# Optimization experiments

Measured on AMD Instinct MI355X. Metric: run time of the kernel, lower is better.

## Reference

```python
import jax, jax.numpy as jnp
import numpy as np

D_MODEL = 1024
D_HIDDEN = 4096
NUM_EXPERTS = 8
TOP_K = 2


def setup_inputs() -> dict:
    key = jax.random.key(0)
    ks = jax.random.split(key, 7)
    scale_in = 1.0 / np.sqrt(D_MODEL)
    scale_hid = 1.0 / np.sqrt(D_HIDDEN)
    x = jax.random.normal(ks[0], (4, 2048, D_MODEL), dtype=jnp.float32)
    Wr = jax.random.uniform(ks[1], (D_MODEL, NUM_EXPERTS), jnp.float32, -scale_in, scale_in)
    br = jax.random.uniform(ks[2], (NUM_EXPERTS,), jnp.float32, -scale_in, scale_in)
    W1 = jax.random.uniform(ks[3], (NUM_EXPERTS, D_MODEL, D_HIDDEN), jnp.float32, -scale_in, scale_in)
    b1 = jax.random.uniform(ks[4], (NUM_EXPERTS, D_HIDDEN), jnp.float32, -scale_in, scale_in)
    W2 = jax.random.uniform(ks[5], (NUM_EXPERTS, D_HIDDEN, D_MODEL), jnp.float32, -scale_hid, scale_hid)
    b2 = jax.random.uniform(ks[6], (NUM_EXPERTS, D_MODEL), jnp.float32, -scale_hid, scale_hid)
    return {"x": x, "Wr": Wr, "br": br, "W1": W1, "b1": b1, "W2": W2, "b2": b2}


def reference(x, Wr, br, W1, b1, W2, b2):
    B, S, D = x.shape
    E = Wr.shape[1]
    flat = x.reshape(-1, D)                      # [T, D]
    T = flat.shape[0]
    logits = flat @ Wr + br                      # [T, E]
    probs = jax.nn.softmax(logits, axis=-1)
    topk_p, topk_i = jax.lax.top_k(probs, TOP_K)  # [T, K]
    topk_p = topk_p / jnp.sum(topk_p, axis=-1, keepdims=True)
    # combine[t, e] = sum_k topk_p[t, k] * (topk_i[t, k] == e)
    combine = jnp.zeros((T, E), flat.dtype).at[jnp.arange(T)[:, None], topk_i].add(topk_p)
    out = jnp.zeros_like(flat)
    for e in range(E):  # fixed small expert loop; each iter is a dense GEMM pair
        h = jax.nn.relu(flat @ W1[e] + b1[e])    # [T, d_hidden]
        y = h @ W2[e] + b2[e]                    # [T, D]
        out = out + y * combine[:, e:e + 1]
    return out.reshape(B, S, D)
```

## Files before the change

### kernel.cpp

```cpp
#include <hip/hip_runtime.h>
#include <stdint.h>

#define D_MODEL  1024
#define D_HIDDEN 4096
#define NE       8
#define T_TOK    8192
#define BM       128
#define BN       128
#define BK       64
#define MAXT     136
#define ROWS_CAP 17408

typedef __attribute__((ext_vector_type(8))) short short8;
typedef __attribute__((ext_vector_type(4))) float f32x4;

__device__ inline uint16_t f2bf(float f) {
  uint32_t u = __float_as_uint(f);
  uint32_t r = (u + 0x7fffu + ((u >> 16) & 1u)) >> 16;
  return (uint16_t)r;
}

#define GLOAD16(gp, lp) __builtin_amdgcn_global_load_lds( \
  (const __attribute__((address_space(1))) uint32_t*)(gp), \
  (__attribute__((address_space(3))) uint32_t*)(lp), 16, 0, 0)

__global__ void transpose_cvt(const float* __restrict__ in, uint16_t* __restrict__ out,
                              int R, int C) {
  __shared__ float tile[64][65];
  size_t eoff = (size_t)blockIdx.z * R * C;
  int c0 = blockIdx.x * 64, r0 = blockIdx.y * 64;
  int t = threadIdx.x;
  int lr = t >> 4, lc4 = (t & 15) * 4;
#pragma unroll
  for (int i = 0; i < 4; ++i) {
    int rr = i * 16 + lr;
    float4 v = *(const float4*)(in + eoff + (size_t)(r0 + rr) * C + c0 + lc4);
    tile[rr][lc4] = v.x; tile[rr][lc4 + 1] = v.y;
    tile[rr][lc4 + 2] = v.z; tile[rr][lc4 + 3] = v.w;
  }
  __syncthreads();
  int oc = t >> 3, orr = (t & 7) * 8;
#pragma unroll
  for (int i = 0; i < 2; ++i) {
    int cc = i * 32 + oc;
    short8 o;
#pragma unroll
    for (int j = 0; j < 8; ++j) o[j] = (short)f2bf(tile[orr + j][cc]);
    *(short8*)(out + eoff + (size_t)(c0 + cc) * R + r0 + orr) = o;
  }
}

__global__ void router_kernel(const float* __restrict__ x, const float* __restrict__ Wr,
                              const float* __restrict__ br,
                              int* __restrict__ cnt, int* __restrict__ tok_of,
                              int* __restrict__ k_of, float* __restrict__ tok_w) {
  int t = blockIdx.x * 4 + (threadIdx.x >> 6);
  int l = threadIdx.x & 63;
  const float* xr = x + (size_t)t * D_MODEL;
  float a[8] = {0.f,0.f,0.f,0.f,0.f,0.f,0.f,0.f};
  for (int d = l; d < D_MODEL; d += 64) {
    float xv = xr[d];
    const float4* w4 = (const float4*)(Wr + d * 8);
    float4 wa = w4[0], wb = w4[1];
    a[0] += xv * wa.x; a[1] += xv * wa.y; a[2] += xv * wa.z; a[3] += xv * wa.w;
    a[4] += xv * wb.x; a[5] += xv * wb.y; a[6] += xv * wb.z; a[7] += xv * wb.w;
  }
#pragma unroll
  for (int e = 0; e < 8; ++e) {
    float v = a[e];
#pragma unroll
    for (int off = 32; off > 0; off >>= 1) v += __shfl_xor(v, off);
    a[e] = v + br[e];
  }
  if (l == 0) {
    int i1 = 0; float v1 = a[0];
#pragma unroll
    for (int e = 1; e < 8; ++e) if (a[e] > v1) { v1 = a[e]; i1 = e; }
    int i2 = -1; float v2 = -1e30f;
#pragma unroll
    for (int e = 0; e < 8; ++e) if (e != i1 && a[e] > v2) { v2 = a[e]; i2 = e; }
    float e2 = __expf(v2 - v1);
    float inv = 1.0f / (1.0f + e2);
    int p1 = atomicAdd(cnt + i1, 1);
    tok_of[i1 * T_TOK + p1] = t; k_of[i1 * T_TOK + p1] = 0;
    int p2 = atomicAdd(cnt + i2, 1);
    tok_of[i2 * T_TOK + p2] = t; k_of[i2 * T_TOK + p2] = 1;
    tok_w[t * 2 + 0] = inv; tok_w[t * 2 + 1] = e2 * inv;
  }
}

__global__ void setup_kernel(const int* __restrict__ cnt, int* __restrict__ meta) {
  int l = threadIdx.x;
  int tiles[8], base[9], tpre[9];
  base[0] = 0; tpre[0] = 0;
#pragma unroll
  for (int e = 0; e < 8; ++e) {
    int c = cnt[e];
    tiles[e] = (c + BM - 1) / BM;
    base[e + 1] = base[e] + tiles[e] * BM;
    tpre[e + 1] = tpre[e] + tiles[e];
  }
  int nt = tpre[8];
  if (l == 0) meta[0] = nt;
  if (l < 9) meta[1 + l] = base[l];
  for (int i = l; i < nt; i += 64) {
    int e = 0;
#pragma unroll
    for (int k = 1; k < 8; ++k) if (i >= tpre[k]) e = k;
    meta[16 + i] = e;
    meta[16 + MAXT + i] = base[e] + (i - tpre[e]) * BM;
  }
}

__global__ void gather_kernel(const float* __restrict__ x, const int* __restrict__ cnt,
                              const int* __restrict__ meta, const int* __restrict__ tok_of,
                              const int* __restrict__ k_of, const float* __restrict__ tok_w,
                              uint16_t* __restrict__ xp,
                              int* __restrict__ row2tok, float* __restrict__ row2w) {
  int r = blockIdx.x * 4 + (threadIdx.x >> 6);
  int l = threadIdx.x & 63;
  int total = meta[9];
  if (r >= total) return;
  int e = 0;
#pragma unroll
  for (int i = 1; i < 8; ++i) if (r >= meta[1 + i]) e = i;
  int p = r - meta[1 + e];
  uint16_t* dst = xp + (size_t)r * D_MODEL + l * 16;
  if (p < cnt[e]) {
    int t = tok_of[e * T_TOK + p];
    if (l == 0) {
      row2tok[r] = t;
      row2w[r] = tok_w[t * 2 + k_of[e * T_TOK + p]];
    }
    const float4* src = (const float4*)(x + (size_t)t * D_MODEL + l * 16);
    short8 o0, o1;
    float4 v0 = src[0], v1 = src[1], v2 = src[2], v3 = src[3];
    o0[0] = (short)f2bf(v0.x); o0[1] = (short)f2bf(v0.y);
    o0[2] = (short)f2bf(v0.z); o0[3] = (short)f2bf(v0.w);
    o0[4] = (short)f2bf(v1.x); o0[5] = (short)f2bf(v1.y);
    o0[6] = (short)f2bf(v1.z); o0[7] = (short)f2bf(v1.w);
    o1[0] = (short)f2bf(v2.x); o1[1] = (short)f2bf(v2.y);
    o1[2] = (short)f2bf(v2.z); o1[3] = (short)f2bf(v2.w);
    o1[4] = (short)f2bf(v3.x); o1[5] = (short)f2bf(v3.y);
    o1[6] = (short)f2bf(v3.z); o1[7] = (short)f2bf(v3.w);
    *(short8*)dst = o0;
    *(short8*)(dst + 8) = o1;
  } else {
    if (l == 0) { row2tok[r] = -1; row2w[r] = 0.f; }
    short8 z = {0,0,0,0,0,0,0,0};
    *(short8*)dst = z;
    *(short8*)(dst + 8) = z;
  }
}

template<int KD, int ND, int NTX, bool FUSED_OUT>
__global__ void moe_gemm(const uint16_t* __restrict__ A, const uint16_t* __restrict__ Bt,
                         const float* __restrict__ bias,
                         uint16_t* __restrict__ Cb, float* __restrict__ out,
                         const int* __restrict__ row2tok, const float* __restrict__ row2w,
                         const int* __restrict__ meta) {
  int nt = meta[0];
  int d = blockIdx.x;
  int xcd = d & 7, q = d >> 3;
  int mt = xcd * (MAXT / 8) + q / NTX;
  if (mt >= nt) return;
  int n0 = (q % NTX) * BN;
  int e = meta[16 + mt];
  int row0 = meta[16 + MAXT + mt];

  __shared__ __align__(16) uint16_t lA[BM * BK];
  __shared__ __align__(16) uint16_t lB[BN * BK];

  int t = threadIdx.x;
  int w = t >> 6, l = t & 63;
  int wr = (w >> 1) * 64, wc = (w & 1) * 64;

  const uint16_t* Ab = A + (size_t)row0 * KD;
  const uint16_t* Bb = Bt + ((size_t)e * ND + n0) * KD;

  f32x4 acc[4][4];
#pragma unroll
  for (int m = 0; m < 4; ++m)
#pragma unroll
    for (int n = 0; n < 4; ++n) acc[m][n] = (f32x4){0.f, 0.f, 0.f, 0.f};

  int trow = t >> 3;
  int tcol = (t & 7) * 8;
  int scol = tcol ^ ((trow & 7) << 3);

  for (int kt = 0; kt < KD / BK; ++kt) {
    int k0 = kt * BK;
    __syncthreads();
#pragma unroll
    for (int i = 0; i < 4; ++i) {
      GLOAD16(Ab + (size_t)(i * 32 + trow) * KD + k0 + scol, lA + (i * 32 + trow) * BK + tcol);
      GLOAD16(Bb + (size_t)(i * 32 + trow) * KD + k0 + scol, lB + (i * 32 + trow) * BK + tcol);
    }
    asm volatile("s_waitcnt vmcnt(0)" ::: "memory");
    __syncthreads();
#pragma unroll
    for (int kk = 0; kk < 2; ++kk) {
      short8 af[4], bf[4];
      int ko = kk * 32 + (l >> 4) * 8;
      int sw = ((l & 7) << 3);
#pragma unroll
      for (int m = 0; m < 4; ++m)
        af[m] = *(const short8*)(lA + (wr + m * 16 + (l & 15)) * BK + (ko ^ sw));
#pragma unroll
      for (int n = 0; n < 4; ++n)
        bf[n] = *(const short8*)(lB + (wc + n * 16 + (l & 15)) * BK + (ko ^ sw));
#pragma unroll
      for (int m = 0; m < 4; ++m)
#pragma unroll
        for (int n = 0; n < 4; ++n)
          acc[m][n] = __builtin_amdgcn_mfma_f32_16x16x32_bf16(af[m], bf[n], acc[m][n], 0, 0, 0);
    }
  }

  if (!FUSED_OUT) {
#pragma unroll
    for (int m = 0; m < 4; ++m) {
      int row_b = row0 + wr + m * 16 + (l >> 4) * 4;
#pragma unroll
      for (int n = 0; n < 4; ++n) {
        int col = n0 + wc + n * 16 + (l & 15);
        float bv = bias[e * ND + col];
#pragma unroll
        for (int r = 0; r < 4; ++r)
          Cb[(size_t)(row_b + r) * ND + col] = f2bf(fmaxf(acc[m][n][r] + bv, 0.f));
      }
    }
  } else {
    float bv[4];
#pragma unroll
    for (int n = 0; n < 4; ++n)
      bv[n] = bias[e * ND + n0 + wc + n * 16 + (l & 15)];
#pragma unroll
    for (int m = 0; m < 4; ++m) {
#pragma unroll
      for (int r = 0; r < 4; ++r) {
        int grow = row0 + wr + m * 16 + (l >> 4) * 4 + r;
        int tok = row2tok[grow];
        float wgt = row2w[grow];
        if (tok >= 0) {
#pragma unroll
          for (int n = 0; n < 4; ++n) {
            int col = n0 + wc + n * 16 + (l & 15);
            atomicAdd(out + (size_t)tok * ND + col, wgt * (acc[m][n][r] + bv[n]));
          }
        }
      }
    }
  }
}

extern "C" void kernel_launch(void* const* d_in, const int* in_sizes, int n_in,
                              void* d_out, int out_size, void* d_ws, size_t ws_size,
                              hipStream_t stream) {
  const float* x  = (const float*)d_in[0];
  const float* Wr = (const float*)d_in[1];
  const float* br = (const float*)d_in[2];
  const float* W1 = (const float*)d_in[3];
  const float* b1 = (const float*)d_in[4];
  const float* W2 = (const float*)d_in[5];
  const float* b2 = (const float*)d_in[6];
  float* out = (float*)d_out;

  char* ws = (char*)d_ws;
  size_t off = 0;
  auto alloc = [&](size_t bytes) -> void* {
    void* p = ws + off;
    off += (bytes + 255) & ~(size_t)255;
    return p;
  };
  uint16_t* W1T    = (uint16_t*)alloc((size_t)NE * D_MODEL * D_HIDDEN * 2);
  uint16_t* W2T    = (uint16_t*)alloc((size_t)NE * D_MODEL * D_HIDDEN * 2);
  uint16_t* xp     = (uint16_t*)alloc((size_t)ROWS_CAP * D_MODEL * 2);
  uint16_t* hp     = (uint16_t*)alloc((size_t)ROWS_CAP * D_HIDDEN * 2);
  int*      cnt    = (int*)alloc(NE * 4);
  int*      tok_of = (int*)alloc((size_t)NE * T_TOK * 4);
  int*      k_of   = (int*)alloc((size_t)NE * T_TOK * 4);
  float*    tok_w  = (float*)alloc(T_TOK * 2 * 4);
  int*      row2tok= (int*)alloc(ROWS_CAP * 4);
  float*    row2w  = (float*)alloc(ROWS_CAP * 4);
  int*      meta   = (int*)alloc((16 + 2 * MAXT) * 4);

  if (ws_size < off) return;

  hipMemsetAsync(cnt, 0, NE * 4, stream);
  hipMemsetAsync(out, 0, (size_t)out_size * 4, stream);
  transpose_cvt<<<dim3(D_HIDDEN / 64, D_MODEL / 64, NE), 256, 0, stream>>>(
      W1, W1T, D_MODEL, D_HIDDEN);
  transpose_cvt<<<dim3(D_MODEL / 64, D_HIDDEN / 64, NE), 256, 0, stream>>>(
      W2, W2T, D_HIDDEN, D_MODEL);
  router_kernel<<<T_TOK / 4, 256, 0, stream>>>(x, Wr, br, cnt, tok_of, k_of, tok_w);
  setup_kernel<<<1, 64, 0, stream>>>(cnt, meta);
  gather_kernel<<<ROWS_CAP / 4, 256, 0, stream>>>(x, cnt, meta, tok_of, k_of, tok_w,
                                                  xp, row2tok, row2w);
  moe_gemm<D_MODEL, D_HIDDEN, 32, false><<<MAXT * 32, 256, 0, stream>>>(
      xp, W1T, b1, hp, nullptr, nullptr, nullptr, meta);
  moe_gemm<D_HIDDEN, D_MODEL, 8, true><<<MAXT * 8, 256, 0, stream>>>(
      hp, W2T, b2, nullptr, out, row2tok, row2w, meta);
}
```

Measured before the change: 691.8 us.

## Double-buffer LDS in MoE GEMM with BK=32 and merge weight transposes

The GEMM main loop moves from a single-buffered BK=64 tile to a double-buffered BK=32 tile. The global-to-LDS load for the next k-step is issued before the MFMAs on the current buffer, so memory latency overlaps compute, and the swizzle is changed to fit the new layout. The two weight transpose/convert launches are also merged into one grid to cut launch overhead and the tail between them. In exchange there are twice as many barriers and k-iterations, each with fewer MFMAs to hide load latency.

```diff
diff --git a/kernel.cpp b/kernel.cpp
--- a/kernel.cpp
+++ b/kernel.cpp
@@ -7,7 +7,6 @@
 #define T_TOK    8192
 #define BM       128
 #define BN       128
-#define BK       64
 #define MAXT     136
 #define ROWS_CAP 17408
 
@@ -24,17 +23,25 @@
   (const __attribute__((address_space(1))) uint32_t*)(gp), \
   (__attribute__((address_space(3))) uint32_t*)(lp), 16, 0, 0)
 
-__global__ void transpose_cvt(const float* __restrict__ in, uint16_t* __restrict__ out,
-                              int R, int C) {
+__global__ void transpose_cvt2(const float* __restrict__ W1, uint16_t* __restrict__ W1T,
+                               const float* __restrict__ W2, uint16_t* __restrict__ W2T) {
   __shared__ float tile[64][65];
-  size_t eoff = (size_t)blockIdx.z * R * C;
-  int c0 = blockIdx.x * 64, r0 = blockIdx.y * 64;
+  int z = blockIdx.z;
+  const float* in; uint16_t* out; int R, C, tx, ty;
+  if (z < 8) {
+    in = W1 + (size_t)z * D_MODEL * D_HIDDEN; out = W1T + (size_t)z * D_MODEL * D_HIDDEN;
+    R = D_MODEL; C = D_HIDDEN; tx = blockIdx.x; ty = blockIdx.y;
+  } else {
+    in = W2 + (size_t)(z - 8) * D_MODEL * D_HIDDEN; out = W2T + (size_t)(z - 8) * D_MODEL * D_HIDDEN;
+    R = D_HIDDEN; C = D_MODEL; tx = blockIdx.x & 15; ty = blockIdx.y * 4 + (blockIdx.x >> 4);
+  }
+  int c0 = tx * 64, r0 = ty * 64;
   int t = threadIdx.x;
   int lr = t >> 4, lc4 = (t & 15) * 4;
 #pragma unroll
   for (int i = 0; i < 4; ++i) {
     int rr = i * 16 + lr;
-    float4 v = *(const float4*)(in + eoff + (size_t)(r0 + rr) * C + c0 + lc4);
+    float4 v = *(const float4*)(in + (size_t)(r0 + rr) * C + c0 + lc4);
     tile[rr][lc4] = v.x; tile[rr][lc4 + 1] = v.y;
     tile[rr][lc4 + 2] = v.z; tile[rr][lc4 + 3] = v.w;
   }
@@ -46,7 +53,7 @@
     short8 o;
 #pragma unroll
     for (int j = 0; j < 8; ++j) o[j] = (short)f2bf(tile[orr + j][cc]);
-    *(short8*)(out + eoff + (size_t)(c0 + cc) * R + r0 + orr) = o;
+    *(short8*)(out + (size_t)(c0 + cc) * R + r0 + orr) = o;
   }
 }
 
@@ -168,8 +175,7 @@
   int e = meta[16 + mt];
   int row0 = meta[16 + MAXT + mt];
 
-  __shared__ __align__(16) uint16_t lA[BM * BK];
-  __shared__ __align__(16) uint16_t lB[BN * BK];
+  __shared__ __align__(16) uint16_t L[16384];
 
   int t = threadIdx.x;
   int w = t >> 6, l = t & 63;
@@ -184,36 +190,45 @@
 #pragma unroll
     for (int n = 0; n < 4; ++n) acc[m][n] = (f32x4){0.f, 0.f, 0.f, 0.f};
 
-  int trow = t >> 3;
-  int tcol = (t & 7) * 8;
-  int scol = tcol ^ ((trow & 7) << 3);
-
-  for (int kt = 0; kt < KD / BK; ++kt) {
-    int k0 = kt * BK;
-    __syncthreads();
-#pragma unroll
-    for (int i = 0; i < 4; ++i) {
-      GLOAD16(Ab + (size_t)(i * 32 + trow) * KD + k0 + scol, lA + (i * 32 + trow) * BK + tcol);
-      GLOAD16(Bb + (size_t)(i * 32 + trow) * KD + k0 + scol, lB + (i * 32 + trow) * BK + tcol);
-    }
-    asm volatile("s_waitcnt vmcnt(0)" ::: "memory");
-    __syncthreads();
-#pragma unroll
-    for (int kk = 0; kk < 2; ++kk) {
-      short8 af[4], bf[4];
-      int ko = kk * 32 + (l >> 4) * 8;
-      int sw = ((l & 7) << 3);
-#pragma unroll
-      for (int m = 0; m < 4; ++m)
-        af[m] = *(const short8*)(lA + (wr + m * 16 + (l & 15)) * BK + (ko ^ sw));
+  int srow = t >> 2;
+  int sseg = ((t & 3) ^ ((srow >> 1) & 3)) * 8;
+  int koff = ((l >> 4) ^ (((l & 15) >> 1) & 3)) * 8;
+
+  auto stage = [&](int buf, int kt) {
+    const uint16_t* ga = Ab + kt * 32;
+    const uint16_t* gb = Bb + kt * 32;
+    uint16_t* ld = L + buf * 8192;
+    GLOAD16(ga + (size_t)srow * KD + sseg, ld + t * 8);
+    GLOAD16(ga + (size_t)(srow + 64) * KD + sseg, ld + 2048 + t * 8);
+    GLOAD16(gb + (size_t)srow * KD + sseg, ld + 4096 + t * 8);
+    GLOAD16(gb + (size_t)(srow + 64) * KD + sseg, ld + 6144 + t * 8);
+  };
+
+  constexpr int NS = KD / 32;
+  stage(0, 0);
+  asm volatile("s_waitcnt vmcnt(0)" ::: "memory");
+  __syncthreads();
+
+  for (int s = 0; s < NS; ++s) {
+    int cur = s & 1;
+    if (s + 1 < NS) stage(cur ^ 1, s + 1);
+    const uint16_t* la = L + cur * 8192;
+    const uint16_t* lb = la + 4096;
+    short8 af[4], bf[4];
+#pragma unroll
+    for (int m = 0; m < 4; ++m)
+      af[m] = *(const short8*)(la + (wr + m * 16 + (l & 15)) * 32 + koff);
+#pragma unroll
+    for (int n = 0; n < 4; ++n)
+      bf[n] = *(const short8*)(lb + (wc + n * 16 + (l & 15)) * 32 + koff);
+#pragma unroll
+    for (int m = 0; m < 4; ++m)
 #pragma unroll
       for (int n = 0; n < 4; ++n)
-        bf[n] = *(const short8*)(lB + (wc + n * 16 + (l & 15)) * BK + (ko ^ sw));
-#pragma unroll
-      for (int m = 0; m < 4; ++m)
-#pragma unroll
-        for (int n = 0; n < 4; ++n)
-          acc[m][n] = __builtin_amdgcn_mfma_f32_16x16x32_bf16(af[m], bf[n], acc[m][n], 0, 0, 0);
+        acc[m][n] = __builtin_amdgcn_mfma_f32_16x16x32_bf16(af[m], bf[n], acc[m][n], 0, 0, 0);
+    if (s + 1 < NS) {
+      asm volatile("s_waitcnt vmcnt(0)" ::: "memory");
+      __syncthreads();
     }
   }
 
@@ -289,10 +304,7 @@
 
   hipMemsetAsync(cnt, 0, NE * 4, stream);
   hipMemsetAsync(out, 0, (size_t)out_size * 4, stream);
-  transpose_cvt<<<dim3(D_HIDDEN / 64, D_MODEL / 64, NE), 256, 0, stream>>>(
-      W1, W1T, D_MODEL, D_HIDDEN);
-  transpose_cvt<<<dim3(D_MODEL / 64, D_HIDDEN / 64, NE), 256, 0, stream>>>(
-      W2, W2T, D_HIDDEN, D_MODEL);
+  transpose_cvt2<<<dim3(64, 16, 16), 256, 0, stream>>>(W1, W1T, W2, W2T);
   router_kernel<<<T_TOK / 4, 256, 0, stream>>>(x, Wr, br, cnt, tok_of, k_of, tok_w);
   setup_kernel<<<1, 64, 0, stream>>>(cnt, meta);
   gather_kernel<<<ROWS_CAP / 4, 256, 0, stream>>>(x, cnt, meta, tok_of, k_of, tok_w,
```

New measurement: 723.0 us. 1.05x slower.
